# Kernel tuning notes

Measured on AMD Instinct MI355X. Metric: run time of the kernel, lower is better.

The kernel has to match this reference:

```python
import jax, jax.numpy as jnp
import numpy as np

TAU = 1.5
K = 4
EPS = 1e-5
GN_GROUPS = 8

def conv2d(x, w, pad, rhs_dilation=(1, 1)):
    return jax.lax.conv_general_dilated(
        x, w, window_strides=(1, 1),
        padding=[(pad, pad), (pad, pad)],
        rhs_dilation=rhs_dilation,
        dimension_numbers=("NCHW", "OIHW", "NCHW"))

def setup_inputs() -> dict:
    key = jax.random.key(0)
    ks = jax.random.split(key, 16)
    s = 0.05  # weight scale to keep activations sane
    B, C, H, W = 16, 128, 64, 64
    O, HID, CG, SE = 128, 32, 16, 16
    d = {}
    d["x"] = jax.random.normal(ks[0], (B, C, H, W), jnp.float32)
    d["base_weight"] = jax.random.normal(ks[1], (O, C, 3, 3), jnp.float32) * s
    d["delta_weight"] = jax.random.normal(ks[2], (K, O, C, 3, 3), jnp.float32) * s
    d["kernel_scale"] = jnp.ones((K, O, 1, 1, 1), jnp.float32)
    d["gc_w1"] = jax.random.normal(ks[3], (HID, C), jnp.float32) * s
    d["gc_w2"] = jax.random.normal(ks[4], (C, HID), jnp.float32) * s
    d["rc_w"] = jax.random.normal(ks[5], (HID, C, 3, 3), jnp.float32) * s
    d["bn_gamma"] = jnp.ones((HID,), jnp.float32)
    d["bn_beta"] = jnp.zeros((HID,), jnp.float32)
    d["bn_mean"] = jnp.zeros((HID,), jnp.float32)
    d["bn_var"] = jnp.ones((HID,), jnp.float32)
    d["rg_w"] = jax.random.normal(ks[6], (HID, C), jnp.float32) * s
    d["gate_w"] = jax.random.normal(ks[7], (K * O, HID), jnp.float32) * s
    d["gate_b"] = jnp.zeros((K * O,), jnp.float32)
    d["cg_w1"] = jax.random.normal(ks[8], (CG, C), jnp.float32) * s
    d["cg_b1"] = jnp.zeros((CG,), jnp.float32)
    d["cg_w2"] = jax.random.normal(ks[9], (C, CG), jnp.float32) * s
    d["cg_b2"] = jnp.zeros((C,), jnp.float32)
    d["sg_w"] = jax.random.normal(ks[10], (1, 2, 7, 7), jnp.float32) * s
    d["gn_gamma"] = jnp.ones((O,), jnp.float32)
    d["gn_beta"] = jnp.zeros((O,), jnp.float32)
    d["se_w1"] = jax.random.normal(ks[11], (SE, O), jnp.float32) * s
    d["se_b1"] = jnp.zeros((SE,), jnp.float32)
    d["se_w2"] = jax.random.normal(ks[12], (O, SE), jnp.float32) * s
    d["se_b2"] = jnp.zeros((O,), jnp.float32)
    d["identity_scale"] = jnp.float32(0.0)
    d["bias"] = jnp.zeros((O,), jnp.float32)
    return d

def reference(x, base_weight, delta_weight, kernel_scale, gc_w1, gc_w2, rc_w,
              bn_gamma, bn_beta, bn_mean, bn_var, rg_w, gate_w, gate_b,
              cg_w1, cg_b1, cg_w2, cg_b2, sg_w, gn_gamma, gn_beta,
              se_w1, se_b1, se_w2, se_b2, identity_scale, bias):
    identity = x
    B, C, H, W = x.shape
    O = base_weight.shape[0]

    # global context gate (squeeze-excite style)
    p = x.mean((2, 3))                                    # [B,C]
    g = jax.nn.sigmoid(jax.nn.silu(p @ gc_w1.T) @ gc_w2.T)
    x = x * g[:, :, None, None]

    # channel gate
    pc = x.mean((2, 3))
    c_attn = jax.nn.sigmoid(jax.nn.silu(pc @ cg_w1.T + cg_b1) @ cg_w2.T + cg_b2)
    # spatial gate
    s_in = jnp.concatenate([x.mean(1, keepdims=True), x.max(1, keepdims=True)], axis=1)
    s_attn = jax.nn.sigmoid(conv2d(s_in, sg_w, pad=3))
    x = x * c_attn[:, :, None, None] * s_attn

    # router: dilated conv + BN(eval) + SiLU, plus global branch
    lf = conv2d(x, rc_w, pad=2, rhs_dilation=(2, 2))
    lf = (lf - bn_mean[None, :, None, None]) * jax.lax.rsqrt(bn_var + EPS)[None, :, None, None]
    lf = lf * bn_gamma[None, :, None, None] + bn_beta[None, :, None, None]
    lf = jax.nn.silu(lf)
    gf = jax.nn.silu(x.mean((2, 3)) @ rg_w.T)             # [B,HID]
    lf = lf + gf[:, :, None, None]
    alpha = jnp.einsum("bhij,oh->boij", lf, gate_w) + gate_b[None, :, None, None]
    alpha = alpha.reshape(B, K, O, H, W)
    alpha = jax.nn.softmax(alpha / TAU, axis=1)

    # unfold (k=3, stride=1, pad=1, dilation=1) -> H_out=H, W_out=W
    xp = jnp.pad(x, ((0, 0), (0, 0), (1, 1), (1, 1)))
    patches = jnp.stack([xp[:, :, i:i + H, j:j + W]
                         for i in range(3) for j in range(3)], axis=2)  # [B,C,9,H,W]
    L = H * W
    xu = patches.reshape(B, C * 9, L).transpose(0, 2, 1)  # [B,L,C*9]

    base = base_weight.reshape(O, -1)
    delta = (delta_weight * kernel_scale).reshape(K, O, -1)
    # same-size bilinear resize of alpha is the identity
    alpha_map = alpha.reshape(B, K, O, L)

    static = jnp.einsum("blf,of->bol", xu, base)          # [B,O,L]
    res = jnp.einsum("blf,kof->bkol", xu, delta)          # [B,K,O,L]
    final = static + (res * alpha_map).sum(1)
    out = final.reshape(B, O, H, W)

    # GroupNorm
    go = out.reshape(B, GN_GROUPS, O // GN_GROUPS, H, W)
    mu = go.mean((2, 3, 4), keepdims=True)
    var = go.var((2, 3, 4), keepdims=True)
    out = ((go - mu) * jax.lax.rsqrt(var + EPS)).reshape(B, O, H, W)
    out = out * gn_gamma[None, :, None, None] + gn_beta[None, :, None, None]

    # output SE
    ps = out.mean((2, 3))
    se = jax.nn.sigmoid(jax.nn.silu(ps @ se_w1.T + se_b1) @ se_w2.T + se_b2)
    out = out * se[:, :, None, None]

    out = out + jnp.tanh(identity_scale) * identity
    out = out + bias[None, :, None, None]
    return out
```

## Files before the change

### kernel.cpp

```cpp
#include <hip/hip_runtime.h>
#include <hip/hip_bf16.h>
#include <math.h>

typedef __bf16 bf16_t;
typedef __bf16 bf16x8 __attribute__((ext_vector_type(8)));
typedef __bf16 bf16x4 __attribute__((ext_vector_type(4)));
typedef float  f32x4  __attribute__((ext_vector_type(4)));

#define EPSF 1e-5f
#define TAUF 1.5f

__device__ __forceinline__ float sigmoidf_(float x){ return 1.f/(1.f+__expf(-x)); }
__device__ __forceinline__ float siluf_(float x){ return x*sigmoidf_(x); }

__device__ __forceinline__ void gload_lds16(const void* g, void* l){
  __builtin_amdgcn_global_load_lds((const __attribute__((address_space(1))) unsigned int*)g,
                                   (__attribute__((address_space(3))) unsigned int*)l, 16, 0, 0);
}

__global__ void k_pool(const float* __restrict__ x, float* __restrict__ p){
  int bc = blockIdx.x; const float* xr = x + (size_t)bc*4096;
  float s = 0.f;
  for (int i = threadIdx.x; i < 4096; i += 256) s += xr[i];
  __shared__ float sb[4];
  for (int off=32; off; off>>=1) s += __shfl_down(s, off);
  if ((threadIdx.x & 63)==0) sb[threadIdx.x>>6] = s;
  __syncthreads();
  if (threadIdx.x==0) p[bc] = (sb[0]+sb[1]+sb[2]+sb[3]) * (1.f/4096.f);
}

__global__ void k_small1(const float* __restrict__ p, const float* __restrict__ gc_w1,
                         const float* __restrict__ gc_w2, const float* __restrict__ cg_w1,
                         const float* __restrict__ cg_b1, const float* __restrict__ cg_w2,
                         const float* __restrict__ cg_b2,
                         float* __restrict__ gbuf, float* __restrict__ gate){
  int b = blockIdx.x; int t = threadIdx.x;
  __shared__ float ps[128], h1[32], pc[128], c1[16];
  ps[t] = p[b*128+t];
  __syncthreads();
  if (t < 32){ float a=0.f; for(int c=0;c<128;c++) a += ps[c]*gc_w1[t*128+c]; h1[t]=siluf_(a); }
  __syncthreads();
  float a=0.f; for(int j=0;j<32;j++) a += h1[j]*gc_w2[t*32+j];
  float g = sigmoidf_(a);
  gbuf[b*128+t] = g; pc[t] = ps[t]*g;
  __syncthreads();
  if (t < 16){ float a2=cg_b1[t]; for(int c=0;c<128;c++) a2 += pc[c]*cg_w1[t*128+c]; c1[t]=siluf_(a2); }
  __syncthreads();
  float a3=cg_b2[t]; for(int j=0;j<16;j++) a3 += c1[j]*cg_w2[t*16+j];
  gate[b*128+t] = g * sigmoidf_(a3);
}

__global__ void k_spatial(const float* __restrict__ x, const float* __restrict__ gbuf,
                          float* __restrict__ sin_){
  int bi = blockIdx.x; int b = bi>>6; int h = bi&63;
  int wv = threadIdx.x>>6, w = threadIdx.x&63;
  __shared__ float psum[4][64], pmax[4][64];
  float sm=0.f, mx=-1e30f;
  const float* xb = x + (((size_t)b*128 + wv*32)*64 + h)*64 + w;
  const float* gb = gbuf + b*128 + wv*32;
  #pragma unroll 4
  for (int c=0;c<32;c++){
    float v = xb[(size_t)c*4096] * gb[c];
    sm += v; mx = fmaxf(mx, v);
  }
  psum[wv][w]=sm; pmax[wv][w]=mx;
  __syncthreads();
  if (threadIdx.x < 64){
    float s = psum[0][w]+psum[1][w]+psum[2][w]+psum[3][w];
    float m = fmaxf(fmaxf(pmax[0][w],pmax[1][w]),fmaxf(pmax[2][w],pmax[3][w]));
    sin_[b*8192 + h*64 + w]        = s*(1.f/128.f);
    sin_[b*8192 + 4096 + h*64 + w] = m;
  }
}

__global__ void __launch_bounds__(256) k_x2(
    const float* __restrict__ x, const float* __restrict__ gate,
    const float* __restrict__ sin_, const float* __restrict__ sg_w,
    bf16_t* __restrict__ x2q, float* __restrict__ pc2){
  int bi = blockIdx.x; int b = bi>>6; int h = bi&63;
  __shared__ float tile[128*65];
  __shared__ float sh_sin[980];
  __shared__ float sh_sgw[98];
  __shared__ float satt_row[64];
  int tid = threadIdx.x, wv = tid>>6, lane = tid&63;
  for (int i=tid;i<980;i+=256){
    int c2 = i/490; int rr = i - c2*490; int r = rr/70; int k = rr - r*70;
    int hh = h + r - 3; int ww = k - 3;
    float v = 0.f;
    if (hh>=0 && hh<64 && ww>=0 && ww<64) v = sin_[b*8192 + c2*4096 + hh*64 + ww];
    sh_sin[i] = v;
  }
  if (tid < 98) sh_sgw[tid] = sg_w[tid];
  __syncthreads();
  if (tid < 64){
    float a = 0.f;
    #pragma unroll
    for (int c2=0;c2<2;c2++)
      #pragma unroll
      for (int r=0;r<7;r++)
        #pragma unroll
        for (int j=0;j<7;j++)
          a += sh_sin[c2*490 + r*70 + tid + j] * sh_sgw[c2*49 + r*7 + j];
    satt_row[tid] = sigmoidf_(a);
  }
  __syncthreads();
  float sa = satt_row[lane];
  const float* xb = x + (((size_t)b*128 + wv*32)*64 + h)*64 + lane;
  const float* gb = gate + b*128 + wv*32;
  #pragma unroll 8
  for (int i=0;i<32;i++)
    tile[(wv*32+i)*65 + lane] = xb[(size_t)i*4096] * gb[i] * sa;
  __syncthreads();
  for (int it=0; it<4; it++){
    int idx = it*256 + tid;
    int cq = idx>>6; int w = idx&63;
    int c0 = cq*8;
    bf16x8 v;
    #pragma unroll
    for (int e=0;e<8;e++) v[e] = (bf16_t)tile[(c0+e)*65 + w];
    *(bf16x8*)(x2q + (((((size_t)b*4 + (cq>>2))*4 + (cq&3))*68 + (h+2))*68 + (w+2))*8) = v;
  }
  if (tid < 128){
    const float* row = &tile[tid*65];
    float s = 0.f;
    #pragma unroll 8
    for (int w=0;w<64;w++) s += row[w];
    atomicAdd(&pc2[b*128+tid], s);
  }
}

__global__ void k_wprep(const float* __restrict__ base_w, const float* __restrict__ delta_w,
                        const float* __restrict__ kscale, const float* __restrict__ rc_w,
                        bf16_t* __restrict__ WCQ, bf16_t* __restrict__ RCWQ,
                        bf16_t* __restrict__ x2q){
  int bx = blockIdx.x;
  if (bx >= 2448){
    int p = bx - 2448;
    size_t base = (size_t)p*68*68*8;
    float4 z = {0.f,0.f,0.f,0.f};
    for (int i = threadIdx.x; i < 272; i += 256){
      int r = i/68; int wp = i - r*68;
      int hp = (r&1) + (r>>1)*66;
      *(float4*)(x2q + base + ((size_t)hp*68 + wp)*8) = z;
    }
    {
      int i = threadIdx.x;
      int hp = 2 + (i>>2);
      int wp = (i&1) + (i&2)*33;
      *(float4*)(x2q + base + ((size_t)hp*68 + wp)*8) = z;
    }
    return;
  }
  int i = bx*256 + threadIdx.x;
  if (i < 589824){
    int c8 = i&7; int o16 = (i>>3)&15; int q = (i>>7)&3; int s = (i>>9)&3;
    int h2 = (i>>11)&3; int r = i>>13; int t = r%9; int ob = r/9;
    int o = ob*16 + o16; int c = h2*32 + q*8 + c8;
    float v = base_w[(o*128+c)*9 + t] + delta_w[(((s*128)+o)*128 + c)*9 + t]*kscale[s*128+o];
    WCQ[i] = (bf16_t)v;
  } else if (i < 589824 + 36864){
    int j = i - 589824;
    int c8 = j&7; int h16 = (j>>3)&15; int q = (j>>7)&3; int n2 = (j>>9)&1;
    int r = j>>10; int t = r%9; int h2 = r/9;
    int hid = n2*16 + h16; int c = h2*32 + q*8 + c8;
    RCWQ[j] = (bf16_t)rc_w[(hid*128+c)*9 + t];
  }
}

__global__ void __launch_bounds__(256) k_router(
    const bf16_t* __restrict__ x2q, const bf16_t* __restrict__ RCWQ,
    const float* __restrict__ bn_gamma, const float* __restrict__ bn_beta,
    const float* __restrict__ bn_mean, const float* __restrict__ bn_var,
    const float* __restrict__ pc2, const float* __restrict__ rg_w,
    bf16_t* __restrict__ lfb){
  __shared__ __align__(16) char smem[44544];
  __shared__ float sgf[32];
  __shared__ float spart[256];
  int tid = threadIdx.x;
  int wv = tid>>6, lane = tid&63, m16 = lane&15, q = lane>>4;
  int rb = blockIdx.x & 31, b = blockIdx.x >> 5;
  int r0 = rb*2;
  int rloc = wv&1;
  int ws0 = (wv>>1)*2;

  {
    int hid = tid&31, seg = tid>>5;
    float a=0.f;
    #pragma unroll
    for (int j=0;j<16;j++) a += pc2[b*128 + seg*16 + j]*rg_w[hid*128 + seg*16 + j];
    spart[tid] = a;
  }

  f32x4 acc[2][2] = {};

  #pragma unroll 1
  for (int h2=0; h2<4; h2++){
    const char* asrc = (const char*)(x2q + ((((size_t)(b*4+h2)*4 + wv)*68 + r0)*68)*8);
    #pragma unroll
    for (int j=0;j<7;j++){
      if (j*64 + lane < 408)
        gload_lds16(asrc + j*1024 + lane*16, (char*)smem + wv*6528 + j*1024);
    }
    const char* wsrc = (const char*)(RCWQ + (size_t)h2*9216) + wv*4608;
    #pragma unroll
    for (int j=0;j<5;j++){
      if (j*64 + lane < 288)
        gload_lds16(wsrc + j*1024 + lane*16, (char*)smem + 26112 + wv*4608 + j*1024);
    }
    __syncthreads();
    if (h2==0 && tid < 32){
      float s = 0.f;
      #pragma unroll
      for (int k=0;k<8;k++) s += spart[k*32+tid];
      sgf[tid] = siluf_(s*(1.f/4096.f));
    }
    #pragma unroll
    for (int t=0; t<9; t++){
      int di = t/3, dj = t - di*3;
      bf16x8 aw0 = *(const bf16x8*)((const char*)smem + 26112 + (t*2+0)*1024 + q*256 + m16*16);
      bf16x8 aw1 = *(const bf16x8*)((const char*)smem + 26112 + (t*2+1)*1024 + q*256 + m16*16);
      #pragma unroll
      for (int mt=0; mt<2; mt++){
        int wseg = ws0 + mt;
        bf16x8 bs = *(const bf16x8*)((const char*)smem + q*6528 +
                     ((rloc + 2*di)*68 + wseg*16 + m16 + 2*dj)*16);
        acc[0][mt] = __builtin_amdgcn_mfma_f32_16x16x32_bf16(aw0, bs, acc[0][mt], 0,0,0);
        acc[1][mt] = __builtin_amdgcn_mfma_f32_16x16x32_bf16(aw1, bs, acc[1][mt], 0,0,0);
      }
    }
    __syncthreads();
  }

  #pragma unroll
  for (int n2=0;n2<2;n2++){
    float aa[4], bb[4];
    #pragma unroll
    for (int i=0;i<4;i++){
      int hid = n2*16 + q*4 + i;
      float a = bn_gamma[hid]*rsqrtf(bn_var[hid]+EPSF);
      aa[i] = a;
      bb[i] = bn_beta[hid] - bn_mean[hid]*a;
    }
    #pragma unroll
    for (int mt=0;mt<2;mt++){
      bf16x4 yv;
      #pragma unroll
      for (int i=0;i<4;i++){
        int hid = n2*16 + q*4 + i;
        yv[i] = (bf16_t)(siluf_(aa[i]*acc[n2][mt][i] + bb[i]) + sgf[hid]);
      }
      size_t pos = (size_t)b*4096 + (r0+rloc)*64 + (ws0+mt)*16 + m16;
      *(bf16x4*)(lfb + pos*32 + n2*16 + q*4) = yv;
    }
  }
}

__global__ void __launch_bounds__(512, 2) k_main(
    const bf16_t* __restrict__ x2q, const bf16_t* __restrict__ WCQ,
    const bf16_t* __restrict__ lfb, const float* __restrict__ gate_w,
    const float* __restrict__ gate_b, bf16_t* __restrict__ outp,
    float* __restrict__ csum, float* __restrict__ cssq){
  __shared__ __align__(16) char smem[161920];
  float* sred = (float*)(smem + 160896);

  int tid = threadIdx.x;
  int wv = tid>>6, lane = tid&63, m16 = lane&15, q = lane>>4;
  int hf = wv>>2, w4 = wv&3;
  int bx = blockIdx.x;
  int ob2 = bx >> 7; int rem = bx & 127; int b = rem >> 3; int hb = rem & 7;
  int h0 = hb*8;
  int obase = (ob2*2 + hf)*16;

  auto STAGE_A = [&](int h2, int bsel){
    int quad = wv>>1, rh = wv&1;
    const char* asrc = (const char*)(x2q + ((((size_t)(b*4+h2)*4 + quad)*68 + (h0+1+rh*5))*68)*8);
    char* adst = (char*)smem + bsel*43584 + quad*10896 + rh*5440;
    #pragma unroll
    for (int j=0;j<6;j++){
      if (j*64 + lane < 340)
        gload_lds16(asrc + (j*64+lane)*16, adst + j*1024);
    }
  };
  auto STAGE_B = [&](int h2){
    int obh = ob2*2 + hf;
    const char* wsrc = (const char*)WCQ + (size_t)(obh*9*4 + h2)*4096;
    char* bdst = (char*)smem + 87168 + hf*36864 + w4*9216;
    #pragma unroll
    for (int j=0;j<9;j++){
      int cc = w4*576 + j*64 + lane;
      int tap = cc>>8, r = cc&255;
      gload_lds16(wsrc + tap*16384 + r*16, bdst + j*1024);
    }
  };

  f32x4 acc[8][4] = {};

  int baseA[8];
  #pragma unroll
  for (int mi=0;mi<8;mi++){
    int row = w4*2 + (mi>>2); int wseg = mi&3;
    baseA[mi] = q*10896 + (row*68 + wseg*16 + m16 + 1)*16;
  }
  int baseB = q*256 + m16*16;

  STAGE_A(0, 0);
  STAGE_B(0);

  #pragma unroll 1
  for (int h2=0; h2<4; h2++){
    if (h2 < 3){
      STAGE_A(h2+1, (h2+1)&1);
      asm volatile("s_waitcnt vmcnt(6)" ::: "memory");
    } else {
      asm volatile("s_waitcnt vmcnt(0)" ::: "memory");
    }
    __builtin_amdgcn_s_barrier();

    const char* Ab = (const char*)smem + (h2&1)*43584;
    const char* Bb = (const char*)smem + 87168 + hf*36864;
    #pragma unroll
    for (int t=0; t<9; t++){
      int di = t/3, dj = t - di*3;
      int toff = (di*68 + dj)*16;
      bf16x8 av[8], bv[4];
      #pragma unroll
      for (int mi=0;mi<8;mi++) av[mi] = *(const bf16x8*)(Ab + baseA[mi] + toff);
      #pragma unroll
      for (int s=0;s<4;s++)  bv[s] = *(const bf16x8*)(Bb + t*4096 + s*1024 + baseB);
      #pragma unroll
      for (int s=0;s<4;s++){
        #pragma unroll
        for (int mi=0;mi<8;mi++)
          acc[mi][s] = __builtin_amdgcn_mfma_f32_16x16x32_bf16(av[mi], bv[s], acc[mi][s], 0,0,0);
      }
    }
    __builtin_amdgcn_s_barrier();
    if (h2 < 3) STAGE_B(h2+1);
  }

  const char* lfsrc = (const char*)(lfb + ((size_t)b*4096 + h0*64)*32);
  #pragma unroll
  for (int j=0;j<4;j++)
    gload_lds16(lfsrc + j*8192 + wv*1024 + lane*16, (char*)smem + j*8192 + wv*1024);
  bf16_t* shGW = (bf16_t*)(smem + 32768);
  for (int idx = tid; idx < 4096; idx += 512){
    int hf2 = idx>>11; int n = (idx>>5)&63; int j2 = idx&31;
    shGW[idx] = (bf16_t)gate_w[((n>>4)*128 + (ob2*2+hf2)*16 + (n&15))*32 + j2];
  }
  __syncthreads();

  bf16x8 bg[4];
  #pragma unroll
  for (int kk=0;kk<4;kk++)
    bg[kk] = *(const bf16x8*)((const char*)shGW + hf*4096 + (kk*16+m16)*64 + q*16);
  float gb[4];
  #pragma unroll
  for (int kk=0;kk<4;kk++) gb[kk] = gate_b[kk*128 + obase + m16];

  const float itau = 1.f/TAUF;
  float s1 = 0.f, s2 = 0.f;
  size_t orow = ((size_t)(b*128 + obase + m16))*4096 + h0*64;
  #pragma unroll
  for (int mi=0; mi<8; mi++){
    bf16x8 avL = *(const bf16x8*)((const char*)smem + (w4*128 + mi*16 + m16)*64 + q*16);
    f32x4 zero = {};
    f32x4 lg[4];
    #pragma unroll
    for (int kk=0;kk<4;kk++)
      lg[kk] = __builtin_amdgcn_mfma_f32_16x16x32_bf16(avL, bg[kk], zero, 0,0,0);
    bf16x4 yv;
    #pragma unroll
    for (int r=0;r<4;r++){
      float l0 = (lg[0][r]+gb[0])*itau, l1 = (lg[1][r]+gb[1])*itau;
      float l2 = (lg[2][r]+gb[2])*itau, l3 = (lg[3][r]+gb[3])*itau;
      float mx = fmaxf(fmaxf(l0,l1),fmaxf(l2,l3));
      float e0=__expf(l0-mx), e1=__expf(l1-mx), e2=__expf(l2-mx), e3=__expf(l3-mx);
      float inv = 1.f/(e0+e1+e2+e3);
      float y = (e0*acc[mi][0][r] + e1*acc[mi][1][r]
               + e2*acc[mi][2][r] + e3*acc[mi][3][r])*inv;
      s1 += y; s2 += y*y;
      yv[r] = (bf16_t)y;
    }
    *(bf16x4*)(outp + orow + w4*128 + mi*16 + q*4) = yv;
  }

  s1 += __shfl_down(s1, 32); s1 += __shfl_down(s1, 16);
  s2 += __shfl_down(s2, 32); s2 += __shfl_down(s2, 16);
  if (lane < 16){ sred[wv*16 + lane] = s1; sred[128 + wv*16 + lane] = s2; }
  __syncthreads();
  if (tid < 32){
    int hf2 = tid>>4, o = tid&15;
    float a = 0.f, c = 0.f;
    #pragma unroll
    for (int k=0;k<4;k++){
      a += sred[(hf2*4+k)*16 + o];
      c += sred[128 + (hf2*4+k)*16 + o];
    }
    atomicAdd(&csum[b*128 + (ob2*2+hf2)*16 + o], a);
    atomicAdd(&cssq[b*128 + (ob2*2+hf2)*16 + o], c);
  }
}

__global__ void k_small3(const float* __restrict__ csum, const float* __restrict__ cssq,
                         const float* __restrict__ gn_gamma, const float* __restrict__ gn_beta,
                         const float* __restrict__ se_w1, const float* __restrict__ se_b1,
                         const float* __restrict__ se_w2, const float* __restrict__ se_b2,
                         float* __restrict__ sca, float* __restrict__ shb){
  int b = blockIdx.x; int o = threadIdx.x;
  __shared__ float s1[128], s2[128], gmu[8], grs[8], psl[128], t1[16];
  s1[o] = csum[b*128+o]; s2[o] = cssq[b*128+o];
  __syncthreads();
  if (o<8){
    float a=0.f,a2=0.f; for(int j=0;j<16;j++){ a+=s1[o*16+j]; a2+=s2[o*16+j]; }
    float mu = a*(1.f/65536.f); float var = a2*(1.f/65536.f) - mu*mu;
    gmu[o]=mu; grs[o]=rsqrtf(var+EPSF);
  }
  __syncthreads();
  int g = o>>4;
  psl[o] = (s1[o]*(1.f/4096.f) - gmu[g])*grs[g]*gn_gamma[o] + gn_beta[o];
  __syncthreads();
  if (o<16){ float a = se_b1[o]; for(int c=0;c<128;c++) a += psl[c]*se_w1[o*128+c]; t1[o]=siluf_(a); }
  __syncthreads();
  float a = se_b2[o]; for(int j=0;j<16;j++) a += t1[j]*se_w2[o*16+j];
  float sev = sigmoidf_(a);
  sca[b*128+o] = grs[g]*gn_gamma[o]*sev;
  shb[b*128+o] = (gn_beta[o] - gmu[g]*grs[g]*gn_gamma[o])*sev;
}

__global__ void k_final(const bf16_t* __restrict__ outp, const float* __restrict__ x,
                        const float* __restrict__ sca, const float* __restrict__ shb,
                        const float* __restrict__ bias, const float* __restrict__ iscale,
                        float* __restrict__ out){
  float ts = tanhf(iscale[0]);
  size_t i = ((size_t)blockIdx.x*256 + threadIdx.x)*8;
  int bo = (int)(i>>12); int o = bo&127;
  float A = sca[bo], Bv = shb[bo] + bias[o];
  bf16x8 ov = *(const bf16x8*)(outp + i);
  float4 x0 = *(const float4*)(x+i), x1 = *(const float4*)(x+i+4);
  float4 r0, r1;
  r0.x = (float)ov[0]*A + Bv + ts*x0.x;
  r0.y = (float)ov[1]*A + Bv + ts*x0.y;
  r0.z = (float)ov[2]*A + Bv + ts*x0.z;
  r0.w = (float)ov[3]*A + Bv + ts*x0.w;
  r1.x = (float)ov[4]*A + Bv + ts*x1.x;
  r1.y = (float)ov[5]*A + Bv + ts*x1.y;
  r1.z = (float)ov[6]*A + Bv + ts*x1.z;
  r1.w = (float)ov[7]*A + Bv + ts*x1.w;
  *(float4*)(out+i) = r0; *(float4*)(out+i+4) = r1;
}

extern "C" void kernel_launch(void* const* d_in, const int* in_sizes, int n_in,
                              void* d_out, int out_size, void* d_ws, size_t ws_size,
                              hipStream_t stream){
  const float* x      = (const float*)d_in[0];
  const float* base_w = (const float*)d_in[1];
  const float* delta_w= (const float*)d_in[2];
  const float* kscale = (const float*)d_in[3];
  const float* gc_w1  = (const float*)d_in[4];
  const float* gc_w2  = (const float*)d_in[5];
  const float* rc_w   = (const float*)d_in[6];
  const float* bn_g   = (const float*)d_in[7];
  const float* bn_b   = (const float*)d_in[8];
  const float* bn_m   = (const float*)d_in[9];
  const float* bn_v   = (const float*)d_in[10];
  const float* rg_w   = (const float*)d_in[11];
  const float* gate_w = (const float*)d_in[12];
  const float* gate_b = (const float*)d_in[13];
  const float* cg_w1  = (const float*)d_in[14];
  const float* cg_b1  = (const float*)d_in[15];
  const float* cg_w2  = (const float*)d_in[16];
  const float* cg_b2  = (const float*)d_in[17];
  const float* sg_w   = (const float*)d_in[18];
  const float* gn_g   = (const float*)d_in[19];
  const float* gn_b   = (const float*)d_in[20];
  const float* se_w1  = (const float*)d_in[21];
  const float* se_b1  = (const float*)d_in[22];
  const float* se_w2  = (const float*)d_in[23];
  const float* se_b2  = (const float*)d_in[24];
  const float* iscale = (const float*)d_in[25];
  const float* bias   = (const float*)d_in[26];
  float* out = (float*)d_out;

  char* ws = (char*)d_ws;
  size_t off = 0;
  auto alloc = [&](size_t bytes)->void*{ void* p = ws + off; off += (bytes + 255) & ~(size_t)255; return p; };
  bf16_t* X2Q = (bf16_t*)alloc(16ull*4*4*68*68*8*2);
  bf16_t* WCQ = (bf16_t*)alloc(589824ull*2);
  bf16_t* RCWQ= (bf16_t*)alloc(36864ull*2);
  bf16_t* LF  = (bf16_t*)alloc(16ull*4096*32*2);
  bf16_t* OUTP= (bf16_t*)alloc(16ull*128*4096*2);
  float* PC2  = (float*)alloc(2048*4);
  float* CSUM = (float*)alloc(2048*4);
  float* CSSQ = (float*)alloc(2048*4);
  float* P    = (float*)alloc(2048*4);
  float* GB   = (float*)alloc(2048*4);
  float* GATE = (float*)alloc(2048*4);
  float* SIN  = (float*)alloc(16ull*8192*4);
  float* SCA  = (float*)alloc(2048*4);
  float* SHB  = (float*)alloc(2048*4);

  (void)hipMemsetAsync(PC2, 0, 3*8192, stream);

  k_wprep  <<<2704, 256, 0, stream>>>(base_w, delta_w, kscale, rc_w, WCQ, RCWQ, X2Q);
  k_pool   <<<2048, 256, 0, stream>>>(x, P);
  k_small1 <<<16,   128, 0, stream>>>(P, gc_w1, gc_w2, cg_w1, cg_b1, cg_w2, cg_b2, GB, GATE);
  k_spatial<<<1024, 256, 0, stream>>>(x, GB, SIN);
  k_x2     <<<1024, 256, 0, stream>>>(x, GATE, SIN, sg_w, X2Q, PC2);
  k_router <<<512,  256, 0, stream>>>(X2Q, RCWQ, bn_g, bn_b, bn_m, bn_v, PC2, rg_w, LF);
  k_main   <<<512,  512, 0, stream>>>(X2Q, WCQ, LF, gate_w, gate_b, OUTP, CSUM, CSSQ);
  k_small3 <<<16,   128, 0, stream>>>(CSUM, CSSQ, gn_g, gn_b, se_w1, se_b1, se_w2, se_b2, SCA, SHB);
  k_final  <<<4096, 256, 0, stream>>>(OUTP, x, SCA, SHB, bias, iscale, out);
}
```

Measured before the change: 263.4 us.

## Pipeline main conv GEMM in tap-row groups with double-buffered weight slices

Splits each channel-chunk iteration of the main conv kernel into three tap-row groups. The weight slices for the next group go into a double buffer that is smaller than the old full 9-tap buffer, and the next A tile is staged in thirds interleaved with compute. This cuts shared memory from about 161KB to 137KB and overlaps B loads with MFMA work instead of loading all B after a barrier. The local-feature load is also moved into the final iteration to overlap with compute, and s_setprio is raised around the MFMA sections. The cost is more barriers and finer-grained vmcnt waits, which must match the issued load counts exactly.

```diff
diff --git a/kernel.cpp b/kernel.cpp
--- a/kernel.cpp
+++ b/kernel.cpp
@@ -260,8 +260,8 @@
     const bf16_t* __restrict__ lfb, const float* __restrict__ gate_w,
     const float* __restrict__ gate_b, bf16_t* __restrict__ outp,
     float* __restrict__ csum, float* __restrict__ cssq){
-  __shared__ __align__(16) char smem[161920];
-  float* sred = (float*)(smem + 160896);
+  __shared__ __align__(16) char smem[137344];
+  float* sred = (float*)(smem + 136320);
 
   int tid = threadIdx.x;
   int wv = tid>>6, lane = tid&63, m16 = lane&15, q = lane>>4;
@@ -271,26 +271,33 @@
   int h0 = hb*8;
   int obase = (ob2*2 + hf)*16;
 
-  auto STAGE_A = [&](int h2, int bsel){
+  auto STAGE_A2 = [&](int h2n, int bsel, int part){
     int quad = wv>>1, rh = wv&1;
-    const char* asrc = (const char*)(x2q + ((((size_t)(b*4+h2)*4 + quad)*68 + (h0+1+rh*5))*68)*8);
+    const char* asrc = (const char*)(x2q + ((((size_t)(b*4+h2n)*4 + quad)*68 + (h0+1+rh*5))*68)*8);
     char* adst = (char*)smem + bsel*43584 + quad*10896 + rh*5440;
     #pragma unroll
-    for (int j=0;j<6;j++){
+    for (int jj=0;jj<2;jj++){
+      int j = part*2+jj;
       if (j*64 + lane < 340)
         gload_lds16(asrc + (j*64+lane)*16, adst + j*1024);
     }
   };
-  auto STAGE_B = [&](int h2){
+  auto STAGE_B3 = [&](int h2n, int gn, int slot){
     int obh = ob2*2 + hf;
-    const char* wsrc = (const char*)WCQ + (size_t)(obh*9*4 + h2)*4096;
-    char* bdst = (char*)smem + 87168 + hf*36864 + w4*9216;
-    #pragma unroll
-    for (int j=0;j<9;j++){
-      int cc = w4*576 + j*64 + lane;
-      int tap = cc>>8, r = cc&255;
-      gload_lds16(wsrc + tap*16384 + r*16, bdst + j*1024);
-    }
+    const char* wsrc = (const char*)WCQ + (size_t)(obh*9 + gn*3)*16384 + (size_t)h2n*4096;
+    char* bdst = (char*)smem + 87168 + slot*24576 + hf*12288;
+    #pragma unroll
+    for (int j=0;j<3;j++){
+      int cc = w4*3 + j;
+      int tl = cc>>2, r = cc&3;
+      gload_lds16(wsrc + tl*16384 + r*1024 + lane*16, bdst + cc*1024);
+    }
+  };
+  auto STAGE_LF = [&](){
+    const char* lfsrc = (const char*)(lfb + ((size_t)b*4096 + h0*64)*32);
+    #pragma unroll
+    for (int j=0;j<4;j++)
+      gload_lds16(lfsrc + j*8192 + wv*1024 + lane*16, (char*)smem + j*8192 + wv*1024);
   };
 
   f32x4 acc[8][4] = {};
@@ -303,45 +310,50 @@
   }
   int baseB = q*256 + m16*16;
 
-  STAGE_A(0, 0);
-  STAGE_B(0);
+  STAGE_A2(0, 0, 0); STAGE_A2(0, 0, 1); STAGE_A2(0, 0, 2);
+  STAGE_B3(0, 0, 0);
 
   #pragma unroll 1
   for (int h2=0; h2<4; h2++){
-    if (h2 < 3){
-      STAGE_A(h2+1, (h2+1)&1);
-      asm volatile("s_waitcnt vmcnt(6)" ::: "memory");
-    } else {
-      asm volatile("s_waitcnt vmcnt(0)" ::: "memory");
-    }
-    __builtin_amdgcn_s_barrier();
-
     const char* Ab = (const char*)smem + (h2&1)*43584;
-    const char* Bb = (const char*)smem + 87168 + hf*36864;
-    #pragma unroll
-    for (int t=0; t<9; t++){
-      int di = t/3, dj = t - di*3;
-      int toff = (di*68 + dj)*16;
-      bf16x8 av[8], bv[4];
+    #pragma unroll
+    for (int g=0; g<3; g++){
+      int slot = (h2 + g) & 1;
+      if (h2 < 3) STAGE_A2(h2+1, (h2+1)&1, g);
+      if (g < 2){
+        STAGE_B3(h2, g+1, slot^1);
+      } else if (h2 < 3){
+        STAGE_B3(h2+1, 0, slot^1);
+      }
+      if (g == 1 && h2 == 3) STAGE_LF();
+      if (h2 < 3)      asm volatile("s_waitcnt vmcnt(5)" ::: "memory");
+      else if (g == 0) asm volatile("s_waitcnt vmcnt(3)" ::: "memory");
+      else if (g == 1) asm volatile("s_waitcnt vmcnt(7)" ::: "memory");
+      else             asm volatile("s_waitcnt vmcnt(0)" ::: "memory");
+      __builtin_amdgcn_s_barrier();
+
+      const char* Bb = (const char*)smem + 87168 + slot*24576 + hf*12288;
+      __builtin_amdgcn_s_setprio(1);
       #pragma unroll
-      for (int mi=0;mi<8;mi++) av[mi] = *(const bf16x8*)(Ab + baseA[mi] + toff);
-      #pragma unroll
-      for (int s=0;s<4;s++)  bv[s] = *(const bf16x8*)(Bb + t*4096 + s*1024 + baseB);
-      #pragma unroll
-      for (int s=0;s<4;s++){
+      for (int tl=0; tl<3; tl++){
+        int toff = g*1088 + tl*16;
+        bf16x8 av[8], bv[4];
         #pragma unroll
-        for (int mi=0;mi<8;mi++)
-          acc[mi][s] = __builtin_amdgcn_mfma_f32_16x16x32_bf16(av[mi], bv[s], acc[mi][s], 0,0,0);
+        for (int mi=0;mi<8;mi++) av[mi] = *(const bf16x8*)(Ab + baseA[mi] + toff);
+        #pragma unroll
+        for (int s=0;s<4;s++)  bv[s] = *(const bf16x8*)(Bb + tl*4096 + s*1024 + baseB);
+        #pragma unroll
+        for (int s=0;s<4;s++){
+          #pragma unroll
+          for (int mi=0;mi<8;mi++)
+            acc[mi][s] = __builtin_amdgcn_mfma_f32_16x16x32_bf16(av[mi], bv[s], acc[mi][s], 0,0,0);
+        }
       }
-    }
-    __builtin_amdgcn_s_barrier();
-    if (h2 < 3) STAGE_B(h2+1);
-  }
-
-  const char* lfsrc = (const char*)(lfb + ((size_t)b*4096 + h0*64)*32);
-  #pragma unroll
-  for (int j=0;j<4;j++)
-    gload_lds16(lfsrc + j*8192 + wv*1024 + lane*16, (char*)smem + j*8192 + wv*1024);
+      __builtin_amdgcn_s_setprio(0);
+      __builtin_amdgcn_s_barrier();
+    }
+  }
+
   bf16_t* shGW = (bf16_t*)(smem + 32768);
   for (int idx = tid; idx < 4096; idx += 512){
     int hf2 = idx>>11; int n = (idx>>5)&63; int j2 = idx&31;
```

Result: slower. 283.2 us (+7.5%).
